# Performance work log

Measured on AMD Instinct MI355X. Metric: run time of the kernel, lower is better.

## Reference

```python
import jax, jax.numpy as jnp
from jax import lax
import numpy as np

B, C, H, W = 32, 256, 56, 56
K = 3
EPS = 1e-5


def setup_inputs() -> dict:
    key = jax.random.key(0)
    k1, k2, k3, k4 = jax.random.split(key, 4)
    x = jax.random.normal(k1, (B, C, H, W), dtype=jnp.float32)
    # xavier_normal init for conv weight [C_out, C_in, K, K]
    fan_in = C * K * K
    fan_out = C * K * K
    std = float(np.sqrt(2.0 / (fan_in + fan_out)))
    w = jax.random.normal(k2, (C, C, K, K), dtype=jnp.float32) * std
    gamma = jnp.ones((C,), dtype=jnp.float32)
    beta = jnp.zeros((C,), dtype=jnp.float32)
    return {"x": x, "w": w, "gamma": gamma, "beta": beta}


def reference(x, w, gamma, beta):
    # --- Binarize (bi_act_method=0, bi_w_scale=1) ---
    bx = jnp.sign(x)                                   # activation sign
    wc = jnp.clip(w, -1.0, 1.0)                        # fp_weight.data.clamp_(-1,1)
    mean_val = jnp.mean(jnp.abs(wc))
    bw = jnp.sign(wc) * mean_val                       # sign(w) * mean(|w|)
    # --- float conv2d, stride 1, padding 1 ---
    out = lax.conv_general_dilated(
        bx, bw, window_strides=(1, 1), padding=[(1, 1), (1, 1)],
        dimension_numbers=("NCHW", "OIHW", "NCHW"))
    # --- identity shortcut (stride=1, C_in==C_out) ---
    out = out + x
    # --- BatchNorm2d (training-mode batch stats, affine) ---
    mean = jnp.mean(out, axis=(0, 2, 3), keepdims=True)
    var = jnp.var(out, axis=(0, 2, 3), keepdims=True)
    out = (out - mean) * lax.rsqrt(var + EPS)
    out = out * gamma[None, :, None, None] + beta[None, :, None, None]
    # --- ReLU ---
    return jax.nn.relu(out)
```

## Files before the change

kernel.cpp:

```cpp
#include <hip/hip_runtime.h>
#include <cstdint>

#define Bn   32
#define Cn   256
#define Hn   56
#define Wn   56
#define HWn  (Hn*Wn)
#define NPIX (Bn*HWn)
#define WELEMS (Cn*Cn*9)
#define EPSv 1e-5f

#define PR   58
#define PPLANE (PR*PR)

#define F_WABS  0
#define F_SUM   64
#define F_SQ    320
#define STATS_BYTES 4096
#define WPK_OFF  4096
#define WPK_BYTES WELEMS
#define ACT_OFF  (WPK_OFF + WPK_BYTES)
#define ACT_BYTES (Bn*PPLANE*Cn)

typedef int v4i __attribute__((ext_vector_type(4)));

__global__ void pack_all(const float* __restrict__ x,
                         const float* __restrict__ w,
                         float* __restrict__ wsf,
                         uint8_t* __restrict__ wpk,
                         uint8_t* __restrict__ act) {
    if (blockIdx.x < 392) {
        int v = blockIdx.x * 256 + threadIdx.x;
        if (v < 7296) {
            int b = v / 228;
            int r = v - b * 228;
            int y, xx;
            if (r < 58)       { y = 0;  xx = r; }
            else if (r < 116) { y = 57; xx = r - 58; }
            else { int r2 = r - 116; y = 1 + (r2 >> 1); xx = (r2 & 1) * 57; }
            uint4* d = (uint4*)(act + ((size_t)(b * PR + y) * PR + xx) * 256);
            uint4 z = make_uint4(0, 0, 0, 0);
            #pragma unroll
            for (int i = 0; i < 16; i++) d[i] = z;
        }
        int b = v / HWn;
        int p = v - b * HWn;
        int y = p / Wn;
        int xx = p - y * Wn;
        const float* xp = x + (size_t)b * Cn * HWn + p;
        int key = (xx + 1) & 15;
        uint32_t* dst = (uint32_t*)(act + ((size_t)(b * PR + (y + 1)) * PR + (xx + 1)) * 256);
        #pragma unroll
        for (int slot = 0; slot < 16; slot++) {
            uint32_t rr[4];
            #pragma unroll
            for (int cw = 0; cw < 4; cw++) {
                uint32_t r = 0;
                #pragma unroll
                for (int j = 0; j < 4; j++) {
                    uint32_t sgn = __float_as_uint(xp[(size_t)(slot * 16 + cw * 4 + j) * HWn]) >> 31;
                    r |= (sgn ? 0xFFu : 0x01u) << (j * 8);
                }
                rr[cw] = r;
            }
            *(uint4*)(dst + (size_t)((slot ^ key) * 4)) = make_uint4(rr[0], rr[1], rr[2], rr[3]);
        }
    } else {
        int u = (blockIdx.x - 392) * 256 + threadIdx.x;
        int co = u / 36;
        int kc = u - co * 36;
        int t  = kc >> 2;
        int s  = kc & 3;
        const float* wp = w + (size_t)co * 2304 + t;
        uint32_t* dst = (uint32_t*)(wpk + ((size_t)kc * 256 + co) * 64);
        float sabs = 0.0f;
        #pragma unroll
        for (int cw = 0; cw < 16; cw++) {
            uint32_t r = 0;
            #pragma unroll
            for (int j = 0; j < 4; j++) {
                int ci = s * 64 + cw * 4 + j;
                float wv = wp[(size_t)ci * 9];
                sabs += fminf(fabsf(wv), 1.0f);
                r |= ((__float_as_uint(wv) >> 31) ? 0xFFu : 0x01u) << (j * 8);
            }
            dst[cw] = r;
        }
        #pragma unroll
        for (int off = 32; off; off >>= 1) sabs += __shfl_down(sabs, off);
        __shared__ float sh[4];
        if ((threadIdx.x & 63) == 0) sh[threadIdx.x >> 6] = sabs;
        __syncthreads();
        if (threadIdx.x == 0)
            atomicAdd(&wsf[F_WABS], sh[0] + sh[1] + sh[2] + sh[3]);
    }
}

__global__ __launch_bounds__(256, 2) void conv_mfma(
    const uint8_t* __restrict__ act, const uint8_t* __restrict__ wpk,
    const float* __restrict__ x, float* __restrict__ wsf,
    float* __restrict__ out) {
    __shared__ uint4 ldsv[3712];
    uint8_t* lds = (uint8_t*)ldsv;

    const int tid  = threadIdx.x;
    const int lane = tid & 63;
    const int wid  = tid >> 6;
    const int l15  = lane & 15;
    const int l4   = lane >> 4;

    const int bx = blockIdx.x;
    const int b  = bx / 28;
    const int y0 = (bx - b * 28) * 2;

    {
        const uint4* src = (const uint4*)(act + ((size_t)b * PR + y0) * PR * 256);
        for (int i = tid; i < 3712; i += 256) ldsv[i] = src[i];
    }

    int pixc[7], cc1[7];
    #pragma unroll
    for (int ni = 0; ni < 7; ni++) {
        int n  = ni * 16 + l15;
        int r_ = n / 56;
        int c_ = n - r_ * 56;
        cc1[ni]  = c_ + 1;
        pixc[ni] = ((r_ + 1) * 58 + (c_ + 1)) * 256;
    }
    const uint8_t* abase = wpk + (wid * 64 + l15) * 64 + l4 * 16;

    v4i af0[4], af1[4], af2[4], af3[4];
    #pragma unroll
    for (int mi = 0; mi < 4; mi++) {
        af0[mi] = *(const v4i*)(abase + (size_t)0 * 16384 + mi * 1024);
        af1[mi] = *(const v4i*)(abase + (size_t)1 * 16384 + mi * 1024);
        af2[mi] = *(const v4i*)(abase + (size_t)2 * 16384 + mi * 1024);
        af3[mi] = *(const v4i*)(abase + (size_t)3 * 16384 + mi * 1024);
    }

    __syncthreads();

    v4i acc[4][7] = {};

#define STEP(S, AF)                                                            \
    {                                                                          \
        v4i bf[7];                                                             \
        _Pragma("unroll")                                                      \
        for (int ni = 0; ni < 7; ni++)                                         \
            bf[ni] = *(const v4i*)(lds + pixb[ni] +                            \
                                   ((((S) * 4 + l4) ^ key[ni]) << 4));         \
        _Pragma("unroll")                                                      \
        for (int ni = 0; ni < 7; ni++) {                                       \
            _Pragma("unroll")                                                  \
            for (int mi = 0; mi < 4; mi++)                                     \
                acc[mi][ni] = __builtin_amdgcn_mfma_i32_16x16x64_i8(           \
                    AF[mi], bf[ni], acc[mi][ni], 0, 0, 0);                     \
        }                                                                      \
        {                                                                      \
            int kcn = t4 + (S) + 4;                                            \
            kcn = kcn > 35 ? 35 : kcn;     \
            const uint8_t* ap = abase + (size_t)kcn * 16384;                   \
            _Pragma("unroll")                                                  \
            for (int mi = 0; mi < 4; mi++)                                     \
                AF[mi] = *(const v4i*)(ap + mi * 1024);                        \
        }                                                                      \
    }

    #pragma unroll 1
    for (int t = 0; t < 9; t++) {
        const int dh = t / 3 - 1;
        const int dw = t % 3 - 1;
        const int toff = (dh * 58 + dw) * 256;
        const int t4 = t * 4;
        int pixb[7], key[7];
        #pragma unroll
        for (int ni = 0; ni < 7; ni++) {
            pixb[ni] = pixc[ni] + toff;
            key[ni]  = (cc1[ni] + dw) & 15;
        }
        STEP(0, af0)
        STEP(1, af1)
        STEP(2, af2)
        STEP(3, af3)
    }
#undef STEP

    const float mv = wsf[F_WABS] * (1.0f / (float)WELEMS);
    const int co_w = wid * 64;
    const int pbase = b * (Cn * HWn) + y0 * 56;

    float ssum[4][4] = {}, ssq[4][4] = {};
    #pragma unroll
    for (int mi = 0; mi < 4; mi++) {
        #pragma unroll
        for (int ni = 0; ni < 7; ni++) {
            v4i a = acc[mi][ni];
            #pragma unroll
            for (int q = 0; q < 4; q++) {
                int co = co_w + mi * 16 + l4 * 4 + q;
                size_t idx = (size_t)pbase + (size_t)co * HWn + (ni * 16 + l15);
                float val = fmaf(mv, (float)a[q], x[idx]);
                out[idx] = val;
                ssum[mi][q] += val;
                ssq[mi][q]  += val * val;
            }
        }
    }
    #pragma unroll
    for (int mi = 0; mi < 4; mi++) {
        #pragma unroll
        for (int q = 0; q < 4; q++) {
            float s = ssum[mi][q], sq = ssq[mi][q];
            #pragma unroll
            for (int off = 1; off < 16; off <<= 1) {
                s  += __shfl_xor(s, off);
                sq += __shfl_xor(sq, off);
            }
            if (l15 == 0) {
                int co = co_w + mi * 16 + l4 * 4 + q;
                atomicAdd(&wsf[F_SUM + co], s);
                atomicAdd(&wsf[F_SQ  + co], sq);
            }
        }
    }
}

__global__ void epilogue_kernel(float* __restrict__ out,
                                const float* __restrict__ wsf,
                                const float* __restrict__ g,
                                const float* __restrict__ bt) {
    int plane = blockIdx.x;
    int c = plane & 255;
    const float n = (float)(Bn * HWn);
    float mean = wsf[F_SUM + c] / n;
    float var  = wsf[F_SQ + c] / n - mean * mean;
    float sc = g[c] * rsqrtf(var + EPSv);
    float sh = bt[c] - mean * sc;
    float4* o4 = (float4*)(out + (size_t)plane * HWn);
    for (int i = threadIdx.x; i < HWn / 4; i += 256) {
        float4 v = o4[i];
        v.x = fmaxf(fmaf(v.x, sc, sh), 0.0f);
        v.y = fmaxf(fmaf(v.y, sc, sh), 0.0f);
        v.z = fmaxf(fmaf(v.z, sc, sh), 0.0f);
        v.w = fmaxf(fmaf(v.w, sc, sh), 0.0f);
        o4[i] = v;
    }
}

extern "C" void kernel_launch(void* const* d_in, const int* in_sizes, int n_in,
                              void* d_out, int out_size, void* d_ws, size_t ws_size,
                              hipStream_t stream) {
    const float* x     = (const float*)d_in[0];
    const float* w     = (const float*)d_in[1];
    const float* gamma = (const float*)d_in[2];
    const float* beta  = (const float*)d_in[3];
    float* out = (float*)d_out;

    float*   wsf = (float*)d_ws;
    uint8_t* wpk = (uint8_t*)d_ws + WPK_OFF;
    uint8_t* act = (uint8_t*)d_ws + ACT_OFF;

    hipMemsetAsync(d_ws, 0, STATS_BYTES, stream);
    pack_all<<<dim3(428), dim3(256), 0, stream>>>(x, w, wsf, wpk, act);
    conv_mfma<<<dim3(896), dim3(256), 0, stream>>>(act, wpk, x, wsf, out);
    epilogue_kernel<<<dim3(Bn * Cn), dim3(256), 0, stream>>>(out, wsf, gamma, beta);
}
```

Baseline: 355.4 us.

## Double-buffer LDS B-fragments and shrink weight-fragment register prefetch

Restructures the inner conv loop so the LDS fragment loads for the next K-step are issued before the MFMAs of the current step, using ping-pong bfA/bfB buffers. The weight fragment prefetch drops from four register sets to two, and per-tap pixel offsets and swizzle keys are now updated incrementally rather than recomputed. The aim is to hide LDS latency behind MFMA work while keeping register pressure similar. The risk is subtle indexing errors across tap boundaries, and the loads issued at the end of the last iteration are wasted.

```diff
diff --git a/kernel.cpp b/kernel.cpp
--- a/kernel.cpp
+++ b/kernel.cpp
@@ -118,47 +118,49 @@
         for (int i = tid; i < 3712; i += 256) ldsv[i] = src[i];
     }
 
-    int pixc[7], cc1[7];
+    const uint8_t* abase = wpk + (wid * 64 + l15) * 64 + l4 * 16;
+
+    v4i af0[4], af1[4];
+    #pragma unroll
+    for (int mi = 0; mi < 4; mi++) {
+        af0[mi] = *(const v4i*)(abase + (size_t)0 * 16384 + mi * 1024);
+        af1[mi] = *(const v4i*)(abase + (size_t)1 * 16384 + mi * 1024);
+    }
+
+    int pixb[7], key[7];
     #pragma unroll
     for (int ni = 0; ni < 7; ni++) {
         int n  = ni * 16 + l15;
         int r_ = n / 56;
         int c_ = n - r_ * 56;
-        cc1[ni]  = c_ + 1;
-        pixc[ni] = ((r_ + 1) * 58 + (c_ + 1)) * 256;
-    }
-    const uint8_t* abase = wpk + (wid * 64 + l15) * 64 + l4 * 16;
-
-    v4i af0[4], af1[4], af2[4], af3[4];
-    #pragma unroll
-    for (int mi = 0; mi < 4; mi++) {
-        af0[mi] = *(const v4i*)(abase + (size_t)0 * 16384 + mi * 1024);
-        af1[mi] = *(const v4i*)(abase + (size_t)1 * 16384 + mi * 1024);
-        af2[mi] = *(const v4i*)(abase + (size_t)2 * 16384 + mi * 1024);
-        af3[mi] = *(const v4i*)(abase + (size_t)3 * 16384 + mi * 1024);
+        pixb[ni] = (r_ * 58 + c_) * 256;
+        key[ni]  = c_ & 15;
     }
 
     __syncthreads();
 
+    v4i bfA[7], bfB[7];
+    #pragma unroll
+    for (int ni = 0; ni < 7; ni++)
+        bfA[ni] = *(const v4i*)(lds + pixb[ni] + ((l4 ^ key[ni]) << 4));
+
     v4i acc[4][7] = {};
 
-#define STEP(S, AF)                                                            \
+#define STEP(SP, BFC, BFN, AF, KCN)                                            \
     {                                                                          \
-        v4i bf[7];                                                             \
         _Pragma("unroll")                                                      \
         for (int ni = 0; ni < 7; ni++)                                         \
-            bf[ni] = *(const v4i*)(lds + pixb[ni] +                            \
-                                   ((((S) * 4 + l4) ^ key[ni]) << 4));         \
+            BFN[ni] = *(const v4i*)(lds + pixb[ni] +                           \
+                                    ((((SP) * 4 + l4) ^ key[ni]) << 4));       \
         _Pragma("unroll")                                                      \
         for (int ni = 0; ni < 7; ni++) {                                       \
             _Pragma("unroll")                                                  \
             for (int mi = 0; mi < 4; mi++)                                     \
                 acc[mi][ni] = __builtin_amdgcn_mfma_i32_16x16x64_i8(           \
-                    AF[mi], bf[ni], acc[mi][ni], 0, 0, 0);                     \
+                    AF[mi], BFC[ni], acc[mi][ni], 0, 0, 0);                    \
         }                                                                      \
         {                                                                      \
-            int kcn = t4 + (S) + 4;                                            \
-            kcn = kcn > 35 ? 35 : kcn;     \
+            int kcn = (KCN) > 35 ? 35 : (KCN);                                 \
             const uint8_t* ap = abase + (size_t)kcn * 16384;                   \
             _Pragma("unroll")                                                  \
             for (int mi = 0; mi < 4; mi++)                                     \
@@ -168,20 +170,20 @@
 
     #pragma unroll 1
     for (int t = 0; t < 9; t++) {
-        const int dh = t / 3 - 1;
-        const int dw = t % 3 - 1;
-        const int toff = (dh * 58 + dw) * 256;
         const int t4 = t * 4;
-        int pixb[7], key[7];
+        const int wrap  = (t == 2 || t == 5);
+        const int dtoff = (t == 8) ? 0 : (wrap ? 56 * 256 : 256);
+        const int ddw   = (t == 8) ? 0 : (wrap ? -2 : 1);
+
+        STEP(1, bfA, bfB, af0, t4 + 2)
+        STEP(2, bfB, bfA, af1, t4 + 3)
+        STEP(3, bfA, bfB, af0, t4 + 4)
         #pragma unroll
         for (int ni = 0; ni < 7; ni++) {
-            pixb[ni] = pixc[ni] + toff;
-            key[ni]  = (cc1[ni] + dw) & 15;
-        }
-        STEP(0, af0)
-        STEP(1, af1)
-        STEP(2, af2)
-        STEP(3, af3)
+            pixb[ni] += dtoff;
+            key[ni]   = (key[ni] + ddw) & 15;
+        }
+        STEP(0, bfB, bfA, af1, t4 + 5)
     }
 #undef STEP
 
```

Measured after the change: 357.6 us. Within noise of the previous version (+0.6%).

## Drop stats memset, use per-block weight partials, load LDS via global_load_lds

Applied to the files above, without the earlier changes.

Removes the hipMemsetAsync by zeroing the BN sum accumulators inside pack_all and by having each weight-pack block write its own |w| partial, which the conv kernel then sums. This drops a launch and the atomic on the weight sum. The conv tile fill now uses direct global-to-LDS loads instead of going through registers. Pixel offsets and swizzle keys are also updated incrementally per tap rather than recomputed. The zeroing of F_SQ stats relies on the layout covering both sum and square arrays in 512 floats; there is a risk if that does not hold.

```diff
diff --git a/kernel.cpp b/kernel.cpp
--- a/kernel.cpp
+++ b/kernel.cpp
@@ -13,16 +13,18 @@
 #define PR   58
 #define PPLANE (PR*PR)
 
-#define F_WABS  0
+#define F_WPART 8
 #define F_SUM   64
 #define F_SQ    320
-#define STATS_BYTES 4096
 #define WPK_OFF  4096
 #define WPK_BYTES WELEMS
 #define ACT_OFF  (WPK_OFF + WPK_BYTES)
 #define ACT_BYTES (Bn*PPLANE*Cn)
 
 typedef int v4i __attribute__((ext_vector_type(4)));
+
+#define GLOBAL_AS __attribute__((address_space(1)))
+#define LDS_AS    __attribute__((address_space(3)))
 
 __global__ void pack_all(const float* __restrict__ x,
                          const float* __restrict__ w,
@@ -30,6 +32,9 @@
                          uint8_t* __restrict__ wpk,
                          uint8_t* __restrict__ act) {
     if (blockIdx.x < 392) {
+        if (blockIdx.x < 2)
+            wsf[F_SUM + blockIdx.x * 256 + threadIdx.x] = 0.0f;
+
         int v = blockIdx.x * 256 + threadIdx.x;
         if (v < 7296) {
             int b = v / 228;
@@ -92,7 +97,7 @@
         if ((threadIdx.x & 63) == 0) sh[threadIdx.x >> 6] = sabs;
         __syncthreads();
         if (threadIdx.x == 0)
-            atomicAdd(&wsf[F_WABS], sh[0] + sh[1] + sh[2] + sh[3]);
+            wsf[F_WPART + (blockIdx.x - 392)] = sh[0] + sh[1] + sh[2] + sh[3];
     }
 }
 
@@ -114,19 +119,19 @@
     const int y0 = (bx - b * 28) * 2;
 
     {
-        const uint4* src = (const uint4*)(act + ((size_t)b * PR + y0) * PR * 256);
-        for (int i = tid; i < 3712; i += 256) ldsv[i] = src[i];
-    }
-
-    int pixc[7], cc1[7];
-    #pragma unroll
-    for (int ni = 0; ni < 7; ni++) {
-        int n  = ni * 16 + l15;
-        int r_ = n / 56;
-        int c_ = n - r_ * 56;
-        cc1[ni]  = c_ + 1;
-        pixc[ni] = ((r_ + 1) * 58 + (c_ + 1)) * 256;
-    }
+        const uint8_t* src = act + ((size_t)b * PR + y0) * PR * 256;
+        #pragma unroll
+        for (int j = 0; j < 15; j++) {
+            int c = wid + j * 4;
+            if (c < 58) {
+                __builtin_amdgcn_global_load_lds(
+                    (const GLOBAL_AS uint32_t*)(const void*)(src + c * 1024 + lane * 16),
+                    (LDS_AS uint32_t*)(void*)(lds + c * 1024),
+                    16, 0, 0);
+            }
+        }
+    }
+
     const uint8_t* abase = wpk + (wid * 64 + l15) * 64 + l4 * 16;
 
     v4i af0[4], af1[4], af2[4], af3[4];
@@ -136,6 +141,16 @@
         af1[mi] = *(const v4i*)(abase + (size_t)1 * 16384 + mi * 1024);
         af2[mi] = *(const v4i*)(abase + (size_t)2 * 16384 + mi * 1024);
         af3[mi] = *(const v4i*)(abase + (size_t)3 * 16384 + mi * 1024);
+    }
+
+    int pixb[7], key[7];
+    #pragma unroll
+    for (int ni = 0; ni < 7; ni++) {
+        int n  = ni * 16 + l15;
+        int r_ = n / 56;
+        int c_ = n - r_ * 56;
+        pixb[ni] = (r_ * 58 + c_) * 256;
+        key[ni]  = c_ & 15;
     }
 
     __syncthreads();
@@ -168,24 +183,27 @@
 
     #pragma unroll 1
     for (int t = 0; t < 9; t++) {
-        const int dh = t / 3 - 1;
-        const int dw = t % 3 - 1;
-        const int toff = (dh * 58 + dw) * 256;
         const int t4 = t * 4;
-        int pixb[7], key[7];
-        #pragma unroll
-        for (int ni = 0; ni < 7; ni++) {
-            pixb[ni] = pixc[ni] + toff;
-            key[ni]  = (cc1[ni] + dw) & 15;
-        }
         STEP(0, af0)
         STEP(1, af1)
         STEP(2, af2)
         STEP(3, af3)
+        const int wrap  = (t == 2 || t == 5);
+        const int dtoff = (t == 8) ? 0 : (wrap ? 56 * 256 : 256);
+        const int ddw   = (t == 8) ? 0 : (wrap ? -2 : 1);
+        #pragma unroll
+        for (int ni = 0; ni < 7; ni++) {
+            pixb[ni] += dtoff;
+            key[ni]   = (key[ni] + ddw) & 15;
+        }
     }
 #undef STEP
 
-    const float mv = wsf[F_WABS] * (1.0f / (float)WELEMS);
+    float wabs = 0.0f;
+    #pragma unroll
+    for (int j = 0; j < 36; j++) wabs += wsf[F_WPART + j];
+    const float mv = wabs * (1.0f / (float)WELEMS);
+
     const int co_w = wid * 64;
     const int pbase = b * (Cn * HWn) + y0 * 56;
 
@@ -260,7 +278,6 @@
     uint8_t* wpk = (uint8_t*)d_ws + WPK_OFF;
     uint8_t* act = (uint8_t*)d_ws + ACT_OFF;
 
-    hipMemsetAsync(d_ws, 0, STATS_BYTES, stream);
     pack_all<<<dim3(428), dim3(256), 0, stream>>>(x, w, wsf, wpk, act);
     conv_mfma<<<dim3(896), dim3(256), 0, stream>>>(act, wpk, x, wsf, out);
     epilogue_kernel<<<dim3(Bn * Cn), dim3(256), 0, stream>>>(out, wsf, gamma, beta);
```

Measured after the change: 346.8 us, median of 2. 2.4% less time.
